# Kernel tuning notes

Measured on AMD Instinct MI355X. Metric: run time of the kernel, lower is better.

Reference implementation:

```python
import jax, jax.numpy as jnp
import numpy as np

NEG_SLOPE = 0.01  # nn.LeakyReLU default used in module

def leaky_relu(x):
    return jnp.where(x >= 0, x, NEG_SLOPE * x)

def setup_inputs() -> dict:
    key = jax.random.key(0)
    k1, k2, k3, k4, k5 = jax.random.split(key, 5)
    B, S, D, H, E = 4, 2048, 1024, 2048, 8
    s_in = 1.0 / np.sqrt(D)
    return {
        "inputs": jax.random.normal(k1, (B, S, D), dtype=jnp.float32),
        "Wg": jax.random.normal(k2, (E, D), dtype=jnp.float32) * s_in,
        "bg": jax.random.normal(k3, (E,), dtype=jnp.float32) * s_in,
        "We": jax.random.normal(k4, (E, H, D), dtype=jnp.float32) * s_in,
        "be": jax.random.normal(k5, (E, H), dtype=jnp.float32) * s_in,
    }

def reference(inputs, Wg, bg, We, be):
    # gate: [B,S,E]
    gate_logits = jnp.einsum('bsd,ed->bse', inputs, Wg) + bg
    gate_probs = jax.nn.softmax(gate_logits, axis=-1)
    # all experts densely: [B,S,E,H]
    expert_out = leaky_relu(jnp.einsum('bsd,ehd->bseh', inputs, We) + be)
    # gate-weighted reduction over experts: [B,S,H]
    weighted = jnp.einsum('bseh,bse->bsh', expert_out, gate_probs)
    return weighted
```

## Files before the change

### kernel.cpp

```cpp
#include <hip/hip_runtime.h>
#include <hip/hip_bf16.h>
#include <math.h>

#define M_TOK 8192
#define N_H   2048
#define K_D   1024
#define N_E   8

typedef __bf16 bf16x8 __attribute__((ext_vector_type(8)));
typedef __bf16 bf16x4 __attribute__((ext_vector_type(4)));
typedef float  f32x4  __attribute__((ext_vector_type(4)));

__device__ inline f32x4 mfma16(bf16x8 a, bf16x8 b, f32x4 c) {
  return __builtin_amdgcn_mfma_f32_16x16x32_bf16(a, b, c, 0, 0, 0);
}

__device__ inline void load16_lds(const void* g, void* l) {
  __builtin_amdgcn_global_load_lds(
      (const __attribute__((address_space(1))) void*)g,
      (__attribute__((address_space(3))) void*)l, 16, 0, 0);
}

__global__ __launch_bounds__(256) void cvt_kernel(const float* __restrict__ src,
                                                  __bf16* __restrict__ dst,
                                                  int n4) {
  int i = blockIdx.x * blockDim.x + threadIdx.x;
  const int stride = gridDim.x * blockDim.x;
  for (; i < n4; i += stride) {
    float4 v = ((const float4*)src)[i];
    bf16x4 o = {(__bf16)v.x, (__bf16)v.y, (__bf16)v.z, (__bf16)v.w};
    *(bf16x4*)(dst + (size_t)i * 4) = o;
  }
}

__global__ __launch_bounds__(256) void gate_kernel(const float* __restrict__ X,
                                                   const float* __restrict__ Wg,
                                                   const float* __restrict__ bg,
                                                   float* __restrict__ gate,
                                                   __bf16* __restrict__ Xb) {
  const int tid = threadIdx.x;
  const int lane = tid & 63;
  const int wv = tid >> 6;
  const int token = blockIdx.x * 4 + wv;
  const float* xrow = X + (size_t)token * K_D;

  float xr[16];
#pragma unroll
  for (int i = 0; i < 16; ++i) xr[i] = xrow[lane + i * 64];

#pragma unroll
  for (int i = 0; i < 16; ++i)
    Xb[(size_t)token * K_D + lane + i * 64] = (__bf16)xr[i];

  float l[N_E];
#pragma unroll
  for (int e = 0; e < N_E; ++e) {
    const float* wrow = Wg + e * K_D;
    float s = 0.f;
#pragma unroll
    for (int i = 0; i < 16; ++i) s += xr[i] * wrow[lane + i * 64];
#pragma unroll
    for (int off = 32; off > 0; off >>= 1) s += __shfl_xor(s, off);
    l[e] = s + bg[e];
  }
  float mx = l[0];
#pragma unroll
  for (int e = 1; e < N_E; ++e) mx = fmaxf(mx, l[e]);
  float p[N_E], den = 0.f;
#pragma unroll
  for (int e = 0; e < N_E; ++e) { p[e] = expf(l[e] - mx); den += p[e]; }
  const float inv = 1.f / den;
  if (lane == 0) {
#pragma unroll
    for (int e = 0; e < N_E; ++e) gate[(size_t)token * N_E + e] = p[e] * inv;
  }
}

__global__ __launch_bounds__(512, 2) void moe_main(
    const __bf16* __restrict__ Xb, const __bf16* __restrict__ Wb,
    const float* __restrict__ gate, const float* __restrict__ be,
    float* __restrict__ out) {
  __shared__ __bf16 As[4][8192];
  __shared__ __bf16 Bs[4][8192];
  __shared__ float gS[256 * 8];
  __shared__ float bS[8 * 128];

  const int tid = threadIdx.x;
  const int lane = tid & 63;
  const int wv = tid >> 6;
  const int wm = wv >> 1;
  const int wn = wv & 1;
  const int row0 = blockIdx.x * 256;
  const int col0 = blockIdx.y * 128;

  for (int i = tid; i < 2048; i += 512) gS[i] = gate[(size_t)row0 * N_E + i];
  for (int i = tid; i < 1024; i += 512)
    bS[i] = be[(size_t)(i >> 7) * N_H + col0 + (i & 127)];

  const int rA = tid >> 2;
  const int kk = (tid & 3) * 8;
  const __bf16* aB = Xb + (size_t)(row0 + rA) * K_D + kk;
  const __bf16* bB = Wb + (size_t)(col0 + rA) * K_D + kk;

  const int lr = lane & 15;
  const int lk = (lane >> 4) * 8;
  const int aOff = (wm * 64 + lr) * 32 + lk;
  const int bOff = (wn * 64 + lr) * 32 + lk;

  f32x4 fin[4][4];
#pragma unroll
  for (int m = 0; m < 4; ++m)
#pragma unroll
    for (int h = 0; h < 4; ++h) fin[m][h] = (f32x4){0.f, 0.f, 0.f, 0.f};

  f32x4 acc[4][8];
#pragma unroll
  for (int m = 0; m < 4; ++m)
#pragma unroll
    for (int n = 0; n < 8; ++n) acc[m][n] = (f32x4){0.f, 0.f, 0.f, 0.f};

  auto STAGE = [&](int sn, int q) {
    const int k0 = (sn & 31) << 5;
    const size_t pOff = (size_t)(sn >> 5) << 22;
    load16_lds(aB + k0, &As[q][tid * 8]);
    load16_lds(aB + (size_t)128 * K_D + k0, &As[q][4096 + tid * 8]);
    load16_lds(bB + pOff + k0, &Bs[q][tid * 8]);
    load16_lds(bB + pOff + (size_t)N_H * K_D + k0, &Bs[q][4096 + tid * 8]);
  };

  auto EPI = [&](int p) {
    const int e0 = p * 2;
#pragma unroll
    for (int m = 0; m < 4; ++m) {
#pragma unroll
      for (int j = 0; j < 4; ++j) {
        const int r = wm * 64 + m * 16 + (lane >> 4) * 4 + j;
        const float g0 = gS[r * 8 + e0];
        const float g1 = gS[r * 8 + e0 + 1];
#pragma unroll
        for (int h = 0; h < 4; ++h) {
          const int c = wn * 64 + h * 16 + lr;
          float v0 = acc[m][h][j] + bS[e0 * 128 + c];
          v0 = (v0 >= 0.f) ? v0 : 0.01f * v0;
          float v1 = acc[m][4 + h][j] + bS[(e0 + 1) * 128 + c];
          v1 = (v1 >= 0.f) ? v1 : 0.01f * v1;
          fin[m][h][j] += g0 * v0 + g1 * v1;
        }
      }
    }
#pragma unroll
    for (int m = 0; m < 4; ++m)
#pragma unroll
      for (int n = 0; n < 8; ++n) acc[m][n] = (f32x4){0.f, 0.f, 0.f, 0.f};
  };

  auto PHASE = [&](int sn, int q, bool doStage, bool lastPhase) {
    if (lastPhase)
      asm volatile("s_waitcnt vmcnt(0)" ::: "memory");
    else
      asm volatile("s_waitcnt vmcnt(4)" ::: "memory");
    __builtin_amdgcn_s_barrier();
    __builtin_amdgcn_sched_barrier(0);

    bf16x8 af[4], bfr[8];
#pragma unroll
    for (int m = 0; m < 4; ++m)
      af[m] = *(const bf16x8*)(&As[q][aOff + m * 512]);
#pragma unroll
    for (int n = 0; n < 8; ++n)
      bfr[n] = *(const bf16x8*)(&Bs[q][bOff + ((n >> 2) * 128 + (n & 3) * 16) * 32]);

    if (doStage) STAGE(sn + 2, (q + 2) & 3);

    __builtin_amdgcn_s_setprio(1);
#pragma unroll
    for (int n = 0; n < 8; ++n)
#pragma unroll
      for (int m = 0; m < 4; ++m)
        acc[m][n] = mfma16(af[m], bfr[n], acc[m][n]);
    __builtin_amdgcn_s_setprio(0);

    if ((sn & 31) == 31) EPI(sn >> 5);
  };

  STAGE(0, 0);
  STAGE(1, 1);

#pragma unroll 1
  for (int t4 = 0; t4 < 31; ++t4) {
    const int sn = t4 * 4;
    PHASE(sn + 0, 0, true, false);
    PHASE(sn + 1, 1, true, false);
    PHASE(sn + 2, 2, true, false);
    PHASE(sn + 3, 3, true, false);
  }
  PHASE(124, 0, true, false);
  PHASE(125, 1, true, false);
  PHASE(126, 2, false, false);
  PHASE(127, 3, false, true);

#pragma unroll
  for (int m = 0; m < 4; ++m) {
#pragma unroll
    for (int j = 0; j < 4; ++j) {
      const size_t r = (size_t)(row0 + wm * 64 + m * 16 + (lane >> 4) * 4 + j);
#pragma unroll
      for (int h = 0; h < 4; ++h) {
        out[r * N_H + col0 + wn * 64 + h * 16 + lr] = fin[m][h][j];
      }
    }
  }
}

extern "C" void kernel_launch(void* const* d_in, const int* in_sizes, int n_in,
                              void* d_out, int out_size, void* d_ws, size_t ws_size,
                              hipStream_t stream) {
  const float* X  = (const float*)d_in[0];
  const float* Wg = (const float*)d_in[1];
  const float* bg = (const float*)d_in[2];
  const float* We = (const float*)d_in[3];
  const float* be = (const float*)d_in[4];
  float* out = (float*)d_out;

  char* ws = (char*)d_ws;
  __bf16* Xb   = (__bf16*)(ws);
  __bf16* Wb   = (__bf16*)(ws + (size_t)16 * 1024 * 1024);
  float*  gate = (float*)(ws + (size_t)48 * 1024 * 1024);

  cvt_kernel<<<2048, 256, 0, stream>>>(We, Wb, (N_E * N_H * K_D) / 4);

  gate_kernel<<<M_TOK / 4, 256, 0, stream>>>(X, Wg, bg, gate, Xb);

  dim3 grid(M_TOK / 256, N_H / 128);
  moe_main<<<grid, 512, 0, stream>>>(Xb, Wb, gate, be, out);
}
```

Measured before the change: 329.4 us.

## Process two K-stages per barrier and split LDS waits across MFMA halves

The main loop now handles two 32-wide K stages per barrier instead of one, which halves the number of workgroup barriers and issues two stages of global-to-LDS prefetch at a time. Within each stage, the LDS fragment reads are overlapped with the first half of the MFMAs using lgkmcnt waits. In exchange, each barrier waits on vmcnt(0), so the prefetch distance drops and the wait sits right after each double phase, which may expose global-load latency.

```diff
diff --git a/kernel.cpp b/kernel.cpp
--- a/kernel.cpp
+++ b/kernel.cpp
@@ -154,50 +154,58 @@
       for (int n = 0; n < 8; ++n) acc[m][n] = (f32x4){0.f, 0.f, 0.f, 0.f};
   };
 
-  auto PHASE = [&](int sn, int q, bool doStage, bool lastPhase) {
-    if (lastPhase)
-      asm volatile("s_waitcnt vmcnt(0)" ::: "memory");
-    else
-      asm volatile("s_waitcnt vmcnt(4)" ::: "memory");
+#define SUBSTEP(qq)                                                          \
+  do {                                                                       \
+    bf16x8 af[4], bfr[8];                                                    \
+    _Pragma("unroll") for (int m = 0; m < 4; ++m)                            \
+        af[m] = *(const bf16x8*)(&As[qq][aOff + m * 512]);                   \
+    _Pragma("unroll") for (int n = 0; n < 8; ++n)                            \
+        bfr[n] = *(const bf16x8*)(                                           \
+            &Bs[qq][bOff + ((n >> 2) * 128 + (n & 3) * 16) * 32]);           \
+    asm volatile("s_waitcnt lgkmcnt(4)" ::: "memory");                       \
+    __builtin_amdgcn_sched_barrier(0);                                       \
+    __builtin_amdgcn_s_setprio(1);                                           \
+    _Pragma("unroll") for (int n = 0; n < 4; ++n)                            \
+        _Pragma("unroll") for (int m = 0; m < 4; ++m)                        \
+            acc[m][n] = mfma16(af[m], bfr[n], acc[m][n]);                    \
+    __builtin_amdgcn_s_setprio(0);                                           \
+    asm volatile("s_waitcnt lgkmcnt(0)" ::: "memory");                       \
+    __builtin_amdgcn_sched_barrier(0);                                       \
+    __builtin_amdgcn_s_setprio(1);                                           \
+    _Pragma("unroll") for (int n = 4; n < 8; ++n)                            \
+        _Pragma("unroll") for (int m = 0; m < 4; ++m)                        \
+            acc[m][n] = mfma16(af[m], bfr[n], acc[m][n]);                    \
+    __builtin_amdgcn_s_setprio(0);                                           \
+  } while (0)
+
+  auto DPHASE = [&](int t, int q, bool doStage) {
+    asm volatile("s_waitcnt vmcnt(0)" ::: "memory");
     __builtin_amdgcn_s_barrier();
     __builtin_amdgcn_sched_barrier(0);
 
-    bf16x8 af[4], bfr[8];
-#pragma unroll
-    for (int m = 0; m < 4; ++m)
-      af[m] = *(const bf16x8*)(&As[q][aOff + m * 512]);
-#pragma unroll
-    for (int n = 0; n < 8; ++n)
-      bfr[n] = *(const bf16x8*)(&Bs[q][bOff + ((n >> 2) * 128 + (n & 3) * 16) * 32]);
-
-    if (doStage) STAGE(sn + 2, (q + 2) & 3);
-
-    __builtin_amdgcn_s_setprio(1);
-#pragma unroll
-    for (int n = 0; n < 8; ++n)
-#pragma unroll
-      for (int m = 0; m < 4; ++m)
-        acc[m][n] = mfma16(af[m], bfr[n], acc[m][n]);
-    __builtin_amdgcn_s_setprio(0);
-
-    if ((sn & 31) == 31) EPI(sn >> 5);
+    if (doStage) {
+      STAGE(2 * t + 2, q ^ 2);
+      STAGE(2 * t + 3, (q ^ 2) + 1);
+    }
+
+    SUBSTEP(q);
+    SUBSTEP(q + 1);
+
+    if ((t & 15) == 15) EPI(t >> 4);
   };
 
   STAGE(0, 0);
   STAGE(1, 1);
 
 #pragma unroll 1
-  for (int t4 = 0; t4 < 31; ++t4) {
-    const int sn = t4 * 4;
-    PHASE(sn + 0, 0, true, false);
-    PHASE(sn + 1, 1, true, false);
-    PHASE(sn + 2, 2, true, false);
-    PHASE(sn + 3, 3, true, false);
-  }
-  PHASE(124, 0, true, false);
-  PHASE(125, 1, true, false);
-  PHASE(126, 2, false, false);
-  PHASE(127, 3, false, true);
+  for (int tp = 0; tp < 31; ++tp) {
+    DPHASE(2 * tp, 0, true);
+    DPHASE(2 * tp + 1, 2, true);
+  }
+  DPHASE(62, 0, true);
+  DPHASE(63, 2, false);
+
+#undef SUBSTEP
 
 #pragma unroll
   for (int m = 0; m < 4; ++m) {
```

Result: no change. 326.1 us (-1.0%).
